# Kernel tuning notes

Measured on AMD Instinct MI355X. Metric: run time of the kernel, lower is better.

## Reference

```python
import jax, jax.numpy as jnp
import numpy as np

B, C, O, H, W = 8, 64, 64, 128, 128


def conv3x3(x, w, b):
    # x: [B,Cin,H,W], w: [Cout,Cin,3,3], stride 1, padding 1
    y = jax.lax.conv_general_dilated(
        x, w, window_strides=(1, 1), padding=((1, 1), (1, 1)),
        dimension_numbers=("NCHW", "OIHW", "NCHW"))
    return y + b[None, :, None, None]


def setup_inputs() -> dict:
    key = jax.random.key(0)
    ks = jax.random.split(key, 6)
    fan = C * 9
    x = jax.random.normal(ks[0], (B, C, H, W), dtype=jnp.float32)
    w_main = jax.random.normal(ks[1], (O, C, 3, 3), dtype=jnp.float32) / np.sqrt(fan)
    # small offset weights keep sampled locations near the regular grid (realistic post-training regime)
    w_offset = jax.random.normal(ks[2], (18, C, 3, 3), dtype=jnp.float32) * 0.05 / np.sqrt(fan)
    b_offset = jnp.zeros((18,), dtype=jnp.float32)
    w_mask = jax.random.normal(ks[3], (9, C, 3, 3), dtype=jnp.float32) / np.sqrt(fan)
    b_mask = jnp.zeros((9,), dtype=jnp.float32)
    return {"x": x, "w_main": w_main, "w_offset": w_offset,
            "b_offset": b_offset, "w_mask": w_mask, "b_mask": b_mask}


def deform_conv2d(x, w_main, offset, mask):
    # torchvision.ops.deform_conv2d: kernel 3x3, stride 1, pad 1, dilation 1, no bias
    Bb, Cc, Hh, Ww = x.shape
    Oo = w_main.shape[0]
    off = offset.reshape(Bb, 9, 2, Hh, Ww)
    dy, dx = off[:, :, 0], off[:, :, 1]            # [B,9,H,W]; pairs ordered (y,x), k row-major
    k = jnp.arange(9)
    kh = (k // 3 - 1).astype(x.dtype)              # kernel row offset in {-1,0,1}
    kw = (k % 3 - 1).astype(x.dtype)
    iy = jnp.arange(Hh, dtype=x.dtype)
    ix = jnp.arange(Ww, dtype=x.dtype)
    # sampling positions p = p0 + p_k + delta_p
    py = dy + iy[None, None, :, None] + kh[None, :, None, None]
    px = dx + ix[None, None, None, :] + kw[None, :, None, None]

    y0 = jnp.floor(py)
    x0 = jnp.floor(px)
    ly = py - y0
    lx = px - x0
    y0i = y0.astype(jnp.int32)
    x0i = x0.astype(jnp.int32)
    y1i = y0i + 1
    x1i = x0i + 1

    bidx = jnp.arange(Bb)[:, None, None, None]

    def corner(yi, xi, wgt):
        # zero-padding semantics: out-of-bounds neighbors contribute 0
        valid = (yi >= 0) & (yi < Hh) & (xi >= 0) & (xi < Ww)
        v = x[bidx, :, jnp.clip(yi, 0, Hh - 1), jnp.clip(xi, 0, Ww - 1)]  # [B,9,H,W,C]
        return v * (wgt * valid)[..., None]

    samp = (corner(y0i, x0i, (1 - ly) * (1 - lx))
            + corner(y0i, x1i, (1 - ly) * lx)
            + corner(y1i, x0i, ly * (1 - lx))
            + corner(y1i, x1i, ly * lx))
    samp = samp * mask[..., None]                  # modulation mask (dcn v2)
    # contract sampled patches with weights: [B,9,H,W,C] x [O,C,9] -> [B,O,H,W]
    return jnp.einsum("bkhwc,ock->bohw", samp, w_main.reshape(Oo, Cc, 9))


def reference(x, w_main, w_offset, b_offset, w_mask, b_mask):
    offset = conv3x3(x, w_offset, b_offset)                 # [B,18,H,W]
    mask = jax.nn.sigmoid(conv3x3(x, w_mask, b_mask))       # [B,9,H,W]
    return deform_conv2d(x, w_main, offset, mask)
```

## Files before the change

kernel.cpp:

```cpp
#include <hip/hip_runtime.h>
#include <math.h>

#define BB 8
#define CC 64
#define OO 64
#define HH 128
#define WW 128
#define HW (HH*WW)
#define NPIX (BB*HW)

typedef __bf16 bf16x8 __attribute__((ext_vector_type(8)));
typedef float floatx4 __attribute__((ext_vector_type(4)));
typedef float f32x2 __attribute__((ext_vector_type(2)));
typedef unsigned short ushort_t;

#define XT_BYTES  16777216
#define OM_BYTES  14680064
#define WT_BYTES  73728

__device__ __forceinline__ unsigned short f2b(float f) {
    unsigned u = __float_as_uint(f);
    u += 0x7fffu + ((u >> 16) & 1u);
    return (unsigned short)(u >> 16);
}

__device__ __forceinline__ unsigned cvt_pk_bf16(float lo, float hi) {
    unsigned r;
    asm("v_cvt_pk_bf16_f32 %0, %1, %2" : "=v"(r) : "v"(lo), "v"(hi));
    return r;
}

__device__ __forceinline__ f32x2 pk_fma(f32x2 a, f32x2 b, f32x2 c) {
    f32x2 d;
    asm("v_pk_fma_f32 %0, %1, %2, %3" : "=v"(d) : "v"(a), "v"(b), "v"(c));
    return d;
}

__device__ __forceinline__ f32x2 pk_mul(f32x2 a, f32x2 b) {
    f32x2 d;
    asm("v_pk_mul_f32 %0, %1, %2" : "=v"(d) : "v"(a), "v"(b));
    return d;
}

__global__ __launch_bounds__(256) void transpose_kernel(
    const float* __restrict__ x, ushort_t* __restrict__ xt)
{
    __shared__ float tile[64][33];
    int bh = blockIdx.x;
    int w0 = blockIdx.y * 32;
    int b  = bh >> 7;
    int h  = bh & 127;
    int t  = threadIdx.x;
    int tx = t & 31;
    int ty = t >> 5;

    #pragma unroll
    for (int j = 0; j < 8; ++j) {
        int c = ty * 8 + j;
        tile[c][tx] = x[(((size_t)(b*CC + c))*HH + h)*WW + (w0 + tx)];
    }
    __syncthreads();
    #pragma unroll
    for (int j = 0; j < 4; ++j) {
        int w  = ty + 8*j;
        int cp = tx;
        unsigned u = cvt_pk_bf16(tile[2*cp][w], tile[2*cp+1][w]);
        *(unsigned*)(xt + (((size_t)(b*HH + h))*WW + (w0 + w))*CC + 2*cp) = u;
    }
}

__global__ __launch_bounds__(256) void repack_kernel(
    const float* __restrict__ wm, const float* __restrict__ woff,
    const float* __restrict__ wmask, ushort_t* __restrict__ wt,
    ushort_t* __restrict__ wb)
{
    int i = blockIdx.x * 256 + threadIdx.x;
    if (i < 36864) {
        int o = i / 576, k = i % 576, tap = k >> 6, c = k & 63;
        wt[i] = f2b(wm[o*576 + c*9 + tap]);
    }
    int j = i - 36864;
    if (j >= 0 && j < 18432) {
        int o = j / 576, k = j % 576, tap = k >> 6, c = k & 63;
        float v = 0.f;
        if (o < 18)      v = woff[o*576 + c*9 + tap];
        else if (o < 27) v = wmask[(o-18)*576 + c*9 + tap];
        wb[j] = f2b(v);
    }
}

__global__ __launch_bounds__(256) void conv27_kernel(
    const ushort_t* __restrict__ xt, const ushort_t* __restrict__ wb,
    const float* __restrict__ boff, const float* __restrict__ bmsk,
    float* __restrict__ om)
{
    __shared__ ushort_t win[10*18*72];
    int bid = blockIdx.x;
    int b  = bid >> 7;
    int th = (bid >> 3) & 15;
    int tw = bid & 7;
    int h0 = th * 8, w0 = tw * 16;
    int t = threadIdx.x;

    for (int idx = t; idx < 10*18*8; idx += 256) {
        int r   = idx / 144;
        int rem = idx - r*144;
        int col = rem >> 3;
        int ch  = (rem & 7) << 3;
        int y = h0 + r - 1, x = w0 + col - 1;
        uint4 val = make_uint4(0,0,0,0);
        if ((unsigned)y < (unsigned)HH && (unsigned)x < (unsigned)WW)
            val = *(const uint4*)(xt + ((((size_t)b*HH + y)*WW + x) << 6) + ch);
        *(uint4*)(win + (r*18 + col)*72 + ch) = val;
    }
    __syncthreads();

    int lane = t & 63, wv = t >> 6;
    int n = lane & 15, quad = lane >> 4;
    const ushort_t* wb0 = wb + n*576;
    const ushort_t* wb1 = wb + (16 + n)*576;

    floatx4 acc0[2], acc1[2];
    #pragma unroll
    for (int mt = 0; mt < 2; ++mt) {
        acc0[mt] = (floatx4){0.f,0.f,0.f,0.f};
        acc1[mt] = (floatx4){0.f,0.f,0.f,0.f};
    }

    #pragma unroll
    for (int s = 0; s < 18; ++s) {
        int tap  = s >> 1;
        int tr   = tap / 3, tc = tap % 3;
        int coff = (s & 1)*32 + quad*8;
        int kk = tap*64 + coff;
        bf16x8 b0 = *(const bf16x8*)(wb0 + kk);
        bf16x8 b1 = *(const bf16x8*)(wb1 + kk);
        #pragma unroll
        for (int mt = 0; mt < 2; ++mt) {
            int ty = wv*2 + mt;
            bf16x8 a = *(const bf16x8*)(win + ((ty + tr)*18 + (n + tc))*72 + coff);
            acc0[mt] = __builtin_amdgcn_mfma_f32_16x16x32_bf16(a, b0, acc0[mt], 0, 0, 0);
            acc1[mt] = __builtin_amdgcn_mfma_f32_16x16x32_bf16(a, b1, acc1[mt], 0, 0, 0);
        }
    }

    #pragma unroll
    for (int mt = 0; mt < 2; ++mt) {
        int ty = wv*2 + mt;
        #pragma unroll
        for (int r = 0; r < 4; ++r) {
            int tx = quad*4 + r;
            size_t p = ((size_t)(b*HH + h0 + ty))*WW + (w0 + tx);
            float* dst = om + p*28;
            dst[n] = acc0[mt][r] + boff[n];
            int o1 = 16 + n;
            if (o1 < 18) {
                dst[o1] = acc1[mt][r] + boff[o1];
            } else if (o1 < 27) {
                float z = acc1[mt][r] + bmsk[o1 - 18];
                dst[o1] = 1.f / (1.f + expf(-z));
            } else if (o1 == 27) {
                dst[27] = 0.f;
            }
        }
    }
}

#define SROW 200

__global__ __launch_bounds__(256, 3) void deform_kernel(
    const ushort_t* __restrict__ xt, const float* __restrict__ om,
    const ushort_t* __restrict__ wt, float* __restrict__ out)
{
    __shared__ ushort_t samp[64*SROW];

    int t = threadIdx.x;
    int lane = t & 63, wv = t >> 6;
    int bid = blockIdx.x;
    int b  = bid >> 8;
    int th = (bid >> 4) & 15;
    int tw = bid & 15;
    int h0 = th * 8, w0 = tw * 8;

    int pa = t >> 2, cg = t & 3;
    int ph = pa >> 3, pw = pa & 7;
    int h_a = h0 + ph, w_a = w0 + pw;
    const float* omp = om + (((size_t)(b*HH + h_a))*WW + w_a) * 28;
    const ushort_t* xbase = xt + ((size_t)b << 20);

    int n = lane & 15, quad = lane >> 4;
    floatx4 acc[4];
    #pragma unroll
    for (int i = 0; i < 4; ++i) acc[i] = (floatx4){0.f,0.f,0.f,0.f};
    const ushort_t* wrow = wt + (wv*16 + n)*576 + quad*8;

    float dyv[3], dxv[3], mv[3];
    #pragma unroll
    for (int j = 0; j < 3; ++j) {
        dyv[j] = omp[2*j]; dxv[j] = omp[2*j+1]; mv[j] = omp[18+j];
    }

    #pragma unroll
    for (int p = 0; p < 3; ++p) {
        bf16x8 wf[6];
        #pragma unroll
        for (int s = 0; s < 6; ++s)
            wf[s] = *(const bf16x8*)(wrow + (p*6 + s)*32);

        #pragma unroll
        for (int kk = 0; kk < 3; ++kk) {
            float py = (float)(h_a + p  - 1) + dyv[kk];
            float px = (float)(w_a + kk - 1) + dxv[kk];
            float y0f = floorf(py), x0f = floorf(px);
            float ly = py - y0f, lx = px - x0f;
            int y0 = (int)y0f, x0 = (int)x0f, y1 = y0 + 1, x1 = x0 + 1;
            float vy0 = ((unsigned)y0 < (unsigned)HH) ? 1.f : 0.f;
            float vy1 = ((unsigned)y1 < (unsigned)HH) ? 1.f : 0.f;
            float vx0 = ((unsigned)x0 < (unsigned)WW) ? 1.f : 0.f;
            float vx1 = ((unsigned)x1 < (unsigned)WW) ? 1.f : 0.f;
            float m   = mv[kk];

            float cw[4] = { (1.f-ly)*(1.f-lx)*vy0*vx0*m,
                            (1.f-ly)*lx      *vy0*vx1*m,
                            ly*(1.f-lx)      *vy1*vx0*m,
                            ly*lx            *vy1*vx1*m };
            int ys[4] = { y0, y0, y1, y1 };
            int xs[4] = { x0, x1, x0, x1 };

            uint4 q[8];
            #pragma unroll
            for (int cn = 0; cn < 4; ++cn) {
                int yc = min(max(ys[cn], 0), HH-1);
                int xc = min(max(xs[cn], 0), WW-1);
                const uint4* cp = (const uint4*)(xbase + (((yc << 7) + xc) << 6) + cg*16);
                q[2*cn]   = cp[0];
                q[2*cn+1] = cp[1];
            }

            f32x2 v2[8];
            {
                f32x2 w2; w2.x = cw[0]; w2.y = cw[0];
                unsigned u0[8] = { q[0].x, q[0].y, q[0].z, q[0].w,
                                   q[1].x, q[1].y, q[1].z, q[1].w };
                #pragma unroll
                for (int j = 0; j < 8; ++j) {
                    f32x2 f;
                    f.x = __uint_as_float(u0[j] << 16);
                    f.y = __uint_as_float(u0[j] & 0xffff0000u);
                    v2[j] = pk_mul(f, w2);
                }
            }
            #pragma unroll
            for (int cn = 1; cn < 4; ++cn) {
                f32x2 w2; w2.x = cw[cn]; w2.y = cw[cn];
                unsigned u0[8] = { q[2*cn].x, q[2*cn].y, q[2*cn].z, q[2*cn].w,
                                   q[2*cn+1].x, q[2*cn+1].y, q[2*cn+1].z, q[2*cn+1].w };
                #pragma unroll
                for (int j = 0; j < 8; ++j) {
                    f32x2 f;
                    f.x = __uint_as_float(u0[j] << 16);
                    f.y = __uint_as_float(u0[j] & 0xffff0000u);
                    v2[j] = pk_fma(f, w2, v2[j]);
                }
            }

            {
                unsigned uu[8];
                #pragma unroll
                for (int j = 0; j < 8; ++j)
                    uu[j] = cvt_pk_bf16(v2[j].x, v2[j].y);
                uint4* dst = (uint4*)(samp + pa*SROW + kk*64 + cg*16);
                dst[0] = make_uint4(uu[0], uu[1], uu[2], uu[3]);
                dst[1] = make_uint4(uu[4], uu[5], uu[6], uu[7]);
            }
        }

        float dyn_[3], dxn_[3], mn_[3];
        if (p < 2) {
            #pragma unroll
            for (int j = 0; j < 3; ++j) {
                int k2 = 3*(p+1) + j;
                dyn_[j] = omp[2*k2]; dxn_[j] = omp[2*k2+1]; mn_[j] = omp[18+k2];
            }
        }

        __syncthreads();

        #pragma unroll
        for (int kk = 0; kk < 3; ++kk) {
            #pragma unroll
            for (int half = 0; half < 2; ++half) {
                bf16x8 bfrag = wf[kk*2 + half];
                #pragma unroll
                for (int mt = 0; mt < 4; ++mt) {
                    bf16x8 afrag = *(const bf16x8*)(samp + (mt*16 + n)*SROW
                                                    + kk*64 + half*32 + quad*8);
                    acc[mt] = __builtin_amdgcn_mfma_f32_16x16x32_bf16(
                                  afrag, bfrag, acc[mt], 0, 0, 0);
                }
            }
        }

        if (p < 2) {
            __syncthreads();
            #pragma unroll
            for (int j = 0; j < 3; ++j) {
                dyv[j] = dyn_[j]; dxv[j] = dxn_[j]; mv[j] = mn_[j];
            }
        }
    }

    float* op = out + ((size_t)b*OO + (wv*16 + n))*HW;
    #pragma unroll
    for (int mt = 0; mt < 4; ++mt) {
        int row = h0 + mt*2 + (quad >> 1);
        int col = w0 + (quad & 1)*4;
        float4 st = make_float4(acc[mt][0], acc[mt][1], acc[mt][2], acc[mt][3]);
        *(float4*)(op + row*WW + col) = st;
    }
}

extern "C" void kernel_launch(void* const* d_in, const int* in_sizes, int n_in,
                              void* d_out, int out_size, void* d_ws, size_t ws_size,
                              hipStream_t stream)
{
    const float* x      = (const float*)d_in[0];
    const float* w_main = (const float*)d_in[1];
    const float* w_off  = (const float*)d_in[2];
    const float* b_off  = (const float*)d_in[3];
    const float* w_msk  = (const float*)d_in[4];
    const float* b_msk  = (const float*)d_in[5];
    float* out = (float*)d_out;

    unsigned char* ws = (unsigned char*)d_ws;
    ushort_t* xt = (ushort_t*)ws;
    float*    om = (float*)(ws + XT_BYTES);
    ushort_t* wt = (ushort_t*)(ws + XT_BYTES + OM_BYTES);
    ushort_t* wb = (ushort_t*)(ws + XT_BYTES + OM_BYTES + WT_BYTES);

    dim3 tgrid(BB*HH, WW/32);
    transpose_kernel<<<tgrid, 256, 0, stream>>>(x, xt);

    repack_kernel<<<(36864 + 18432 + 255)/256, 256, 0, stream>>>(
        w_main, w_off, w_msk, wt, wb);

    conv27_kernel<<<NPIX/128, 256, 0, stream>>>(xt, wb, b_off, b_msk, om);

    deform_kernel<<<NPIX/64, 256, 0, stream>>>(xt, om, wt, out);
}
```

Measured before the change: 162.0 us.

## Fuse offset/mask conv into deform kernel and merge prep kernels

The transpose and weight-repack kernels are merged into one launch, cutting the pipeline from four launches to two. The 27-channel offset/mask convolution now runs inside the deform kernel on each 8x8 tile, using a 10x10 haloed window in shared memory. Its results go to shared memory instead of a global om buffer, which removes that buffer's write and read traffic. In exchange, halo pixels are loaded redundantly, occupancy is raised to 4 blocks per SM, and the shared scratch is reused for the window, so it depends on a later barrier before the sample buffer is overwritten.

Result: no change. 164.7 us (+1.6%).

```diff
diff --git a/kernel.cpp b/kernel.cpp
--- a/kernel.cpp
+++ b/kernel.cpp
@@ -42,137 +42,67 @@
     return d;
 }
 
-__global__ __launch_bounds__(256) void transpose_kernel(
-    const float* __restrict__ x, ushort_t* __restrict__ xt)
+__global__ __launch_bounds__(256) void prep_kernel(
+    const float* __restrict__ x,
+    const float* __restrict__ wm, const float* __restrict__ woff,
+    const float* __restrict__ wmask,
+    ushort_t* __restrict__ xt, ushort_t* __restrict__ wt,
+    ushort_t* __restrict__ wb)
 {
     __shared__ float tile[64][33];
-    int bh = blockIdx.x;
-    int w0 = blockIdx.y * 32;
-    int b  = bh >> 7;
-    int h  = bh & 127;
-    int t  = threadIdx.x;
-    int tx = t & 31;
-    int ty = t >> 5;
-
-    #pragma unroll
-    for (int j = 0; j < 8; ++j) {
-        int c = ty * 8 + j;
-        tile[c][tx] = x[(((size_t)(b*CC + c))*HH + h)*WW + (w0 + tx)];
-    }
-    __syncthreads();
-    #pragma unroll
-    for (int j = 0; j < 4; ++j) {
-        int w  = ty + 8*j;
-        int cp = tx;
-        unsigned u = cvt_pk_bf16(tile[2*cp][w], tile[2*cp+1][w]);
-        *(unsigned*)(xt + (((size_t)(b*HH + h))*WW + (w0 + w))*CC + 2*cp) = u;
-    }
-}
-
-__global__ __launch_bounds__(256) void repack_kernel(
-    const float* __restrict__ wm, const float* __restrict__ woff,
-    const float* __restrict__ wmask, ushort_t* __restrict__ wt,
-    ushort_t* __restrict__ wb)
-{
-    int i = blockIdx.x * 256 + threadIdx.x;
-    if (i < 36864) {
-        int o = i / 576, k = i % 576, tap = k >> 6, c = k & 63;
-        wt[i] = f2b(wm[o*576 + c*9 + tap]);
-    }
-    int j = i - 36864;
-    if (j >= 0 && j < 18432) {
-        int o = j / 576, k = j % 576, tap = k >> 6, c = k & 63;
-        float v = 0.f;
-        if (o < 18)      v = woff[o*576 + c*9 + tap];
-        else if (o < 27) v = wmask[(o-18)*576 + c*9 + tap];
-        wb[j] = f2b(v);
-    }
-}
-
-__global__ __launch_bounds__(256) void conv27_kernel(
+    int bid = blockIdx.x;
+    int t   = threadIdx.x;
+
+    if (bid < 4096) {
+        int bh = bid >> 2;
+        int w0 = (bid & 3) * 32;
+        int b  = bh >> 7;
+        int h  = bh & 127;
+        int tx = t & 31;
+        int ty = t >> 5;
+
+        #pragma unroll
+        for (int j = 0; j < 8; ++j) {
+            int c = ty * 8 + j;
+            tile[c][tx] = x[(((size_t)(b*CC + c))*HH + h)*WW + (w0 + tx)];
+        }
+        __syncthreads();
+        #pragma unroll
+        for (int j = 0; j < 4; ++j) {
+            int w  = ty + 8*j;
+            int cp = tx;
+            unsigned u = cvt_pk_bf16(tile[2*cp][w], tile[2*cp+1][w]);
+            *(unsigned*)(xt + (((size_t)(b*HH + h))*WW + (w0 + w))*CC + 2*cp) = u;
+        }
+    } else {
+        int i = (bid - 4096) * 256 + t;
+        if (i < 36864) {
+            int o = i / 576, k = i % 576, tap = k >> 6, c = k & 63;
+            wt[i] = f2b(wm[o*576 + c*9 + tap]);
+        }
+        int j = i - 36864;
+        if (j >= 0 && j < 18432) {
+            int o = j / 576, k = j % 576, tap = k >> 6, c = k & 63;
+            float v = 0.f;
+            if (o < 18)      v = woff[o*576 + c*9 + tap];
+            else if (o < 27) v = wmask[(o-18)*576 + c*9 + tap];
+            wb[j] = f2b(v);
+        }
+    }
+}
+
+#define SROW 200
+#define WROW 72
+
+__global__ __launch_bounds__(256, 4) void conv_deform_kernel(
     const ushort_t* __restrict__ xt, const ushort_t* __restrict__ wb,
     const float* __restrict__ boff, const float* __restrict__ bmsk,
-    float* __restrict__ om)
-{
-    __shared__ ushort_t win[10*18*72];
-    int bid = blockIdx.x;
-    int b  = bid >> 7;
-    int th = (bid >> 3) & 15;
-    int tw = bid & 7;
-    int h0 = th * 8, w0 = tw * 16;
-    int t = threadIdx.x;
-
-    for (int idx = t; idx < 10*18*8; idx += 256) {
-        int r   = idx / 144;
-        int rem = idx - r*144;
-        int col = rem >> 3;
-        int ch  = (rem & 7) << 3;
-        int y = h0 + r - 1, x = w0 + col - 1;
-        uint4 val = make_uint4(0,0,0,0);
-        if ((unsigned)y < (unsigned)HH && (unsigned)x < (unsigned)WW)
-            val = *(const uint4*)(xt + ((((size_t)b*HH + y)*WW + x) << 6) + ch);
-        *(uint4*)(win + (r*18 + col)*72 + ch) = val;
-    }
-    __syncthreads();
-
-    int lane = t & 63, wv = t >> 6;
-    int n = lane & 15, quad = lane >> 4;
-    const ushort_t* wb0 = wb + n*576;
-    const ushort_t* wb1 = wb + (16 + n)*576;
-
-    floatx4 acc0[2], acc1[2];
-    #pragma unroll
-    for (int mt = 0; mt < 2; ++mt) {
-        acc0[mt] = (floatx4){0.f,0.f,0.f,0.f};
-        acc1[mt] = (floatx4){0.f,0.f,0.f,0.f};
-    }
-
-    #pragma unroll
-    for (int s = 0; s < 18; ++s) {
-        int tap  = s >> 1;
-        int tr   = tap / 3, tc = tap % 3;
-        int coff = (s & 1)*32 + quad*8;
-        int kk = tap*64 + coff;
-        bf16x8 b0 = *(const bf16x8*)(wb0 + kk);
-        bf16x8 b1 = *(const bf16x8*)(wb1 + kk);
-        #pragma unroll
-        for (int mt = 0; mt < 2; ++mt) {
-            int ty = wv*2 + mt;
-            bf16x8 a = *(const bf16x8*)(win + ((ty + tr)*18 + (n + tc))*72 + coff);
-            acc0[mt] = __builtin_amdgcn_mfma_f32_16x16x32_bf16(a, b0, acc0[mt], 0, 0, 0);
-            acc1[mt] = __builtin_amdgcn_mfma_f32_16x16x32_bf16(a, b1, acc1[mt], 0, 0, 0);
-        }
-    }
-
-    #pragma unroll
-    for (int mt = 0; mt < 2; ++mt) {
-        int ty = wv*2 + mt;
-        #pragma unroll
-        for (int r = 0; r < 4; ++r) {
-            int tx = quad*4 + r;
-            size_t p = ((size_t)(b*HH + h0 + ty))*WW + (w0 + tx);
-            float* dst = om + p*28;
-            dst[n] = acc0[mt][r] + boff[n];
-            int o1 = 16 + n;
-            if (o1 < 18) {
-                dst[o1] = acc1[mt][r] + boff[o1];
-            } else if (o1 < 27) {
-                float z = acc1[mt][r] + bmsk[o1 - 18];
-                dst[o1] = 1.f / (1.f + expf(-z));
-            } else if (o1 == 27) {
-                dst[27] = 0.f;
-            }
-        }
-    }
-}
-
-#define SROW 200
-
-__global__ __launch_bounds__(256, 3) void deform_kernel(
-    const ushort_t* __restrict__ xt, const float* __restrict__ om,
     const ushort_t* __restrict__ wt, float* __restrict__ out)
 {
     __shared__ ushort_t samp[64*SROW];
+    __shared__ float om_lds[64][28];
+
+    ushort_t* win = samp;
 
     int t = threadIdx.x;
     int lane = t & 63, wv = t >> 6;
@@ -182,13 +112,64 @@
     int tw = bid & 15;
     int h0 = th * 8, w0 = tw * 8;
 
+    const ushort_t* xbase = xt + ((size_t)b << 20);
+    int n = lane & 15, quad = lane >> 4;
+
+    for (int idx = t; idx < 800; idx += 256) {
+        int cell = idx >> 3;
+        int ch   = (idx & 7) << 3;
+        int cy = cell / 10, cx = cell - cy*10;
+        int y = h0 + cy - 1, xx = w0 + cx - 1;
+        uint4 val = make_uint4(0,0,0,0);
+        if ((unsigned)y < (unsigned)HH && (unsigned)xx < (unsigned)WW)
+            val = *(const uint4*)(xbase + (((y << 7) + xx) << 6) + ch);
+        *(uint4*)(win + cell*WROW + ch) = val;
+    }
+    __syncthreads();
+
+    {
+        int p   = wv*16 + n;
+        int cph = p >> 3, cpw = p & 7;
+        const ushort_t* wb0 = wb + n*576;
+        const ushort_t* wb1 = wb + (16 + n)*576;
+        floatx4 c0 = (floatx4){0.f,0.f,0.f,0.f};
+        floatx4 c1 = (floatx4){0.f,0.f,0.f,0.f};
+
+        #pragma unroll
+        for (int s = 0; s < 18; ++s) {
+            int tap  = s >> 1;
+            int tr   = tap / 3, tc = tap % 3;
+            int coff = (s & 1)*32 + quad*8;
+            bf16x8 b0 = *(const bf16x8*)(wb0 + tap*64 + coff);
+            bf16x8 b1 = *(const bf16x8*)(wb1 + tap*64 + coff);
+            bf16x8 a  = *(const bf16x8*)(win + ((cph + tr)*10 + (cpw + tc))*WROW + coff);
+            c0 = __builtin_amdgcn_mfma_f32_16x16x32_bf16(a, b0, c0, 0, 0, 0);
+            c1 = __builtin_amdgcn_mfma_f32_16x16x32_bf16(a, b1, c1, 0, 0, 0);
+        }
+
+        #pragma unroll
+        for (int r = 0; r < 4; ++r) {
+            int p_out = wv*16 + quad*4 + r;
+            float* dst = &om_lds[p_out][0];
+            dst[n] = c0[r] + boff[n];
+            int o1 = 16 + n;
+            if (o1 < 18) {
+                dst[o1] = c1[r] + boff[o1];
+            } else if (o1 < 27) {
+                float z = c1[r] + bmsk[o1 - 18];
+                dst[o1] = 1.f / (1.f + expf(-z));
+            } else if (o1 == 27) {
+                dst[27] = 0.f;
+            }
+        }
+    }
+    __syncthreads();
+
     int pa = t >> 2, cg = t & 3;
     int ph = pa >> 3, pw = pa & 7;
     int h_a = h0 + ph, w_a = w0 + pw;
-    const float* omp = om + (((size_t)(b*HH + h_a))*WW + w_a) * 28;
-    const ushort_t* xbase = xt + ((size_t)b << 20);
-
-    int n = lane & 15, quad = lane >> 4;
+    const float* omp = &om_lds[pa][0];
+
     floatx4 acc[4];
     #pragma unroll
     for (int i = 0; i < 4; ++i) acc[i] = (floatx4){0.f,0.f,0.f,0.f};
@@ -334,17 +315,10 @@
 
     unsigned char* ws = (unsigned char*)d_ws;
     ushort_t* xt = (ushort_t*)ws;
-    float*    om = (float*)(ws + XT_BYTES);
     ushort_t* wt = (ushort_t*)(ws + XT_BYTES + OM_BYTES);
     ushort_t* wb = (ushort_t*)(ws + XT_BYTES + OM_BYTES + WT_BYTES);
 
-    dim3 tgrid(BB*HH, WW/32);
-    transpose_kernel<<<tgrid, 256, 0, stream>>>(x, xt);
-
-    repack_kernel<<<(36864 + 18432 + 255)/256, 256, 0, stream>>>(
-        w_main, w_off, w_msk, wt, wb);
-
-    conv27_kernel<<<NPIX/128, 256, 0, stream>>>(xt, wb, b_off, b_msk, om);
-
-    deform_kernel<<<NPIX/64, 256, 0, stream>>>(xt, om, wt, out);
-}
+    prep_kernel<<<4096 + 216, 256, 0, stream>>>(x, w_main, w_off, w_msk, xt, wt, wb);
+
+    conv_deform_kernel<<<NPIX/64, 256, 0, stream>>>(xt, wb, b_off, b_msk, wt, out);
+}
```
